# Optimization experiments

Measured on AMD Instinct MI355X. Metric: run time of the kernel, lower is better.

The kernel has to match this reference:

```python
import jax, jax.numpy as jnp
import numpy as np

DIM = 1024
NUM_HEADS = 16
HEAD_DIM = DIM // NUM_HEADS
SCALE = HEAD_DIM ** -0.5


def setup_inputs() -> dict:
    key = jax.random.key(0)
    k1, k2, k3, k4, k5 = jax.random.split(key, 5)
    B, N = 2, 2048
    h = jax.random.normal(k1, (B, N, DIM), dtype=jnp.float32)
    mask = jax.random.uniform(k2, (B, N), dtype=jnp.float32)  # non-negative, sqrt-safe
    # nn.Linear(dim, dim*3, bias=False): weight applied as x @ W^T; store as [dim, 3*dim]
    w_qkv = jax.random.normal(k3, (DIM, 3 * DIM), dtype=jnp.float32) * (DIM ** -0.5)
    w_proj = jax.random.normal(k4, (DIM, DIM), dtype=jnp.float32) * (DIM ** -0.5)
    b_proj = jax.random.normal(k5, (DIM,), dtype=jnp.float32) * 0.01
    return {"h": h, "mask": mask, "w_qkv": w_qkv, "w_proj": w_proj, "b_proj": b_proj}


def reference(h, mask, w_qkv, w_proj, b_proj):
    B, N, C = h.shape
    H, D = NUM_HEADS, HEAD_DIM
    # qkv projection -> [3, B, H, N, D]
    qkv = (h @ w_qkv).reshape(B, N, 3, H, D).transpose(2, 0, 3, 1, 4)
    q, k, v = qkv[0], qkv[1], qkv[2]
    # scores [B,H,N,N]; scale applied to logits (same math as (q@k^T)*scale)
    attn = jax.nn.softmax(jnp.einsum('bhqd,bhkd->bhqk', q, k) * SCALE, axis=-1)
    # post-softmax multiplicative mask over the KEY dimension: mask[B,N]->[B,1,1,N]
    attn = attn * mask[:, None, None, :]
    new_mask = jnp.sqrt(mask)
    out = jnp.einsum('bhqk,bhkd->bhqd', attn, v)          # [B,H,N,D]
    out = out.transpose(0, 2, 1, 3).reshape(B, N, C)       # [B,N,C]
    out = out @ w_proj + b_proj
    return out, new_mask
```

## Files before the change

kernel.cpp:

```cpp
#include <hip/hip_runtime.h>
#include <hip/hip_bf16.h>
#include <math.h>

#define DIMC   1024
#define NHEADS 16
#define HDIM   64
#define BATCH  2
#define SEQ    2048
#define SCALE  0.125f
#define QSCL   (0.125f * 1.44269504088896341f)

typedef unsigned short u16;
typedef unsigned int   u32;
typedef __attribute__((ext_vector_type(8))) short bf16x8;
typedef _Float16 f16x8 __attribute__((ext_vector_type(8)));
typedef __attribute__((ext_vector_type(4))) float f32x4;

#define BHND ((size_t)BATCH * NHEADS * SEQ * HDIM)
#define MROWS ((size_t)BATCH * SEQ)

__device__ __forceinline__ u16 f2bf(float x) {
    __hip_bfloat16 h = __float2bfloat16(x);
    return *reinterpret_cast<u16*>(&h);
}
__device__ __forceinline__ u16 f2h(float x) {
    _Float16 h = (_Float16)x;
    return *reinterpret_cast<u16*>(&h);
}
__device__ __forceinline__ u32 cvt_pk_bf16(float a, float b) {
    u32 r;
    asm("v_cvt_pk_bf16_f32 %0, %1, %2" : "=v"(r) : "v"(a), "v"(b));
    return r;
}
__device__ __forceinline__ void gload_lds16(const u16* g, u16* l) {
    __builtin_amdgcn_global_load_lds(
        (const __attribute__((address_space(1))) unsigned int*)g,
        (__attribute__((address_space(3))) unsigned int*)l, 16, 0, 0);
}

__global__ __launch_bounds__(256) void prep_h_kernel(
    const float* __restrict__ in, u16* __restrict__ outh)
{
    int i = (blockIdx.x * 256 + threadIdx.x) * 8;
    float4 a = *(const float4*)&in[i];
    float4 b = *(const float4*)&in[i + 4];
    float v[8] = {a.x, a.y, a.z, a.w, b.x, b.y, b.z, b.w};
    bf16x8 o;
    #pragma unroll
    for (int j = 0; j < 8; ++j) o[j] = (short)f2h(v[j]);
    *(bf16x8*)&outh[i] = o;
}

__global__ __launch_bounds__(256) void prep_w_kernel(
    const float* __restrict__ W, u16* __restrict__ T, int K, int N)
{
    __shared__ float Ws[64][65];
    const int kb  = blockIdx.x * 64;
    const int nb  = blockIdx.y * 64;
    const int tid = threadIdx.x;
    const int jr  = (tid & 15) * 4;
    const int ir  = tid >> 4;
    #pragma unroll
    for (int it = 0; it < 4; ++it) {
        int i = ir + it * 16;
        *(float4*)&Ws[i][jr] = *(const float4*)&W[(size_t)(kb + i) * N + nb + jr];
    }
    __syncthreads();
    const int n  = tid >> 2;
    const int k0 = (tid & 3) * 16;
    bf16x8 h0, h1;
    #pragma unroll
    for (int kk = 0; kk < 8; ++kk) {
        h0[kk] = (short)f2h(Ws[k0 + kk][n]);
        h1[kk] = (short)f2h(Ws[k0 + 8 + kk][n]);
    }
    size_t off = (size_t)(nb + n) * K + kb + k0;
    *(bf16x8*)&T[off]     = h0;
    *(bf16x8*)&T[off + 8] = h1;
}

template <int MODE>
__global__ __launch_bounds__(256) void gemm_f16_kernel(
    const u16* __restrict__ A, const u16* __restrict__ B,
    const float* __restrict__ bias, const float* __restrict__ vmask,
    float* __restrict__ outf, u16* __restrict__ outb,
    int M, int N, int K)
{
    __shared__ __align__(16) u16 lds[2][128 * 32];

    const int bm   = blockIdx.y * 128;
    const int bn   = blockIdx.x * 128;
    const int tid  = threadIdx.x;
    const int wid  = tid >> 6;
    const int lane = tid & 63;
    const int lo   = lane & 15;
    const int g4   = lane >> 4;
    const int wr   = wid >> 1, wc = wid & 1;

    const int mrow = lane >> 2;
    const int ks8  = (lane & 3) * 8;
    const u16* g0  = (wid < 2)
        ? A + (size_t)(bm + (wid & 1) * 64 + mrow) * K + ks8
        : B + (size_t)(bn + (wid & 1) * 64 + mrow) * K + ks8;
    u16* lbase = &lds[wid >> 1][(wid & 1) * 64 * 32];

    f32x4 acc[4][4] = {};

    for (int k0 = 0; k0 < K; k0 += 32) {
        const u16* g = g0 + k0;
        #pragma unroll
        for (int s = 0; s < 4; ++s)
            gload_lds16(g + (size_t)s * 16 * K, lbase + s * 512);
        __syncthreads();

        f16x8 bfr[4];
        #pragma unroll
        for (int ni = 0; ni < 4; ++ni)
            bfr[ni] = *(const f16x8*)&lds[1][(wc * 64 + ni * 16 + lo) * 32 + g4 * 8];
        #pragma unroll
        for (int mi = 0; mi < 4; ++mi) {
            f16x8 a = *(const f16x8*)&lds[0][(wr * 64 + mi * 16 + lo) * 32 + g4 * 8];
            #pragma unroll
            for (int ni = 0; ni < 4; ++ni)
                acc[mi][ni] = __builtin_amdgcn_mfma_f32_16x16x32_f16(a, bfr[ni], acc[mi][ni], 0, 0, 0);
        }
        __syncthreads();
    }

    if (MODE == 0) {
        #pragma unroll
        for (int mi = 0; mi < 4; ++mi) {
            int m0 = bm + wr * 64 + mi * 16 + 4 * g4;
            #pragma unroll
            for (int ni = 0; ni < 4; ++ni) {
                int n0    = bn + wc * 64 + ni * 16;
                int which = n0 >> 10;
                int head  = (n0 & 1023) >> 6;
                int d     = (n0 & 63) + lo;
                if (which == 0) {
                    #pragma unroll
                    for (int r = 0; r < 4; ++r) {
                        int m = m0 + r, b = m >> 11, seq = m & 2047;
                        outb[(((size_t)b * NHEADS + head) * SEQ + seq) * HDIM + d] =
                            f2bf(acc[mi][ni][r] * QSCL);
                    }
                } else if (which == 1) {
                    #pragma unroll
                    for (int r = 0; r < 4; ++r) {
                        int m = m0 + r, b = m >> 11, seq = m & 2047;
                        outb[BHND + (((size_t)b * NHEADS + head) * SEQ + seq) * HDIM + d] =
                            f2bf(acc[mi][ni][r]);
                    }
                } else {
                    int b = m0 >> 11, seq0 = m0 & 2047;
                    float4 mv = *(const float4*)&vmask[b * SEQ + seq0];
                    ushort4 o;
                    o.x = f2bf(acc[mi][ni][0] * mv.x);
                    o.y = f2bf(acc[mi][ni][1] * mv.y);
                    o.z = f2bf(acc[mi][ni][2] * mv.z);
                    o.w = f2bf(acc[mi][ni][3] * mv.w);
                    *(ushort4*)&outb[2 * BHND +
                        (((size_t)b * NHEADS + head) * HDIM + d) * SEQ + seq0] = o;
                }
            }
        }
    } else {
        #pragma unroll
        for (int ni = 0; ni < 4; ++ni) {
            int col = bn + wc * 64 + ni * 16 + lo;
            float bv = bias[col];
            #pragma unroll
            for (int mi = 0; mi < 4; ++mi) {
                int m0 = bm + wr * 64 + mi * 16 + 4 * g4;
                #pragma unroll
                for (int r = 0; r < 4; ++r)
                    outf[(size_t)(m0 + r) * N + col] = acc[mi][ni][r] + bv;
            }
        }
    }
}

__global__ __launch_bounds__(256) void attn_mfma_kernel(
    const u16* __restrict__ qb, const u16* __restrict__ kb,
    const u16* __restrict__ vtb, u16* __restrict__ oA)
{
    __shared__ __align__(16) u16 Ks[64 * 64];
    __shared__ __align__(16) u16 Vt[64 * 64];
    __shared__ __align__(16) u16 Plds[4][16 * 72];

    const int bid  = blockIdx.x;
    const int qt   = bid & 31;
    const int h    = (bid >> 5) & 15;
    const int b    = bid >> 9;
    const int tid  = threadIdx.x;
    const int wid  = tid >> 6;
    const int lane = tid & 63;
    const int lo   = lane & 15;
    const int g    = lane >> 4;

    const size_t bh = (size_t)b * NHEADS + h;
    const int qbase = qt * 64 + wid * 16;

    const u16* qrowp = qb + (bh * SEQ + qbase + lo) * HDIM + 8 * g;
    const bf16x8 aq0 = *(const bf16x8*)(qrowp);
    const bf16x8 aq1 = *(const bf16x8*)(qrowp + 32);

    const int srow  = tid >> 2;
    const int scol  = (tid & 3) * 16;
    const int swz   = (srow & 7) << 3;
    const int idx0  = srow * 64 + (scol ^ swz);
    const int idx1  = srow * 64 + ((scol + 8) ^ swz);
    const u16* kgp  = kb  + (bh * SEQ  + srow) * HDIM + scol;
    const u16* vgp  = vtb + (bh * HDIM + srow) * SEQ  + scol;

    int kof0[4], kof1[4];
    #pragma unroll
    for (int kt = 0; kt < 4; ++kt) {
        int key  = lo + 16 * kt;
        int kbse = key * 64;
        int ksw  = (key & 7) << 3;
        kof0[kt] = kbse + ((8 * g) ^ ksw);
        kof1[kt] = kbse + ((32 + 8 * g) ^ ksw);
    }
    int vof0[4], vof1[4];
    #pragma unroll
    for (int dt = 0; dt < 4; ++dt) {
        int vbse = (lo + 16 * dt) * 64;
        int vsw  = (lo & 7) << 3;
        vof0[dt] = vbse + ((8 * g) ^ vsw);
        vof1[dt] = vbse + ((32 + 8 * g) ^ vsw);
    }

    bf16x8 ones;
    #pragma unroll
    for (int j = 0; j < 8; ++j) ones[j] = (short)0x3F80;

    f32x4 acc[4] = {};
    f32x4 accl = {};

    u16* pw = &Plds[wid][0];

    bf16x8 rk0 = *(const bf16x8*)(kgp);
    bf16x8 rk1 = *(const bf16x8*)(kgp + 8);
    bf16x8 rv0 = *(const bf16x8*)(vgp);
    bf16x8 rv1 = *(const bf16x8*)(vgp + 8);

    for (int k0 = 0; k0 < SEQ; k0 += 64) {
        __syncthreads();
        *(bf16x8*)&Ks[idx0] = rk0;
        *(bf16x8*)&Ks[idx1] = rk1;
        *(bf16x8*)&Vt[idx0] = rv0;
        *(bf16x8*)&Vt[idx1] = rv1;
        __syncthreads();
        if (k0 + 64 < SEQ) {
            const u16* kn = kgp + (size_t)(k0 + 64) * HDIM;
            rk0 = *(const bf16x8*)(kn);
            rk1 = *(const bf16x8*)(kn + 8);
            rv0 = *(const bf16x8*)(vgp + k0 + 64);
            rv1 = *(const bf16x8*)(vgp + k0 + 64 + 8);
        }

        f32x4 s[4];
        #pragma unroll
        for (int kt = 0; kt < 4; ++kt) {
            f32x4 t = {};
            t = __builtin_amdgcn_mfma_f32_16x16x32_bf16(*(const bf16x8*)&Ks[kof0[kt]], aq0, t, 0, 0, 0);
            t = __builtin_amdgcn_mfma_f32_16x16x32_bf16(*(const bf16x8*)&Ks[kof1[kt]], aq1, t, 0, 0, 0);
            s[kt] = t;
        }

        #pragma unroll
        for (int kt = 0; kt < 4; ++kt) {
            uint2 pr;
            pr.x = cvt_pk_bf16(__builtin_amdgcn_exp2f(s[kt][0]),
                               __builtin_amdgcn_exp2f(s[kt][1]));
            pr.y = cvt_pk_bf16(__builtin_amdgcn_exp2f(s[kt][2]),
                               __builtin_amdgcn_exp2f(s[kt][3]));
            *(uint2*)&pw[lo * 72 + 16 * kt + 4 * g] = pr;
        }

        const bf16x8 pa0 = *(const bf16x8*)&pw[lo * 72 + 8 * g];
        const bf16x8 pa1 = *(const bf16x8*)&pw[lo * 72 + 32 + 8 * g];
        accl = __builtin_amdgcn_mfma_f32_16x16x32_bf16(pa0, ones, accl, 0, 0, 0);
        accl = __builtin_amdgcn_mfma_f32_16x16x32_bf16(pa1, ones, accl, 0, 0, 0);
        #pragma unroll
        for (int dt = 0; dt < 4; ++dt) {
            acc[dt] = __builtin_amdgcn_mfma_f32_16x16x32_bf16(pa0, *(const bf16x8*)&Vt[vof0[dt]], acc[dt], 0, 0, 0);
            acc[dt] = __builtin_amdgcn_mfma_f32_16x16x32_bf16(pa1, *(const bf16x8*)&Vt[vof1[dt]], acc[dt], 0, 0, 0);
        }
    }

    #pragma unroll
    for (int r = 0; r < 4; ++r) {
        float invq = 1.f / accl[r];
        size_t row = (size_t)b * SEQ + qbase + 4 * g + r;
        u16* dst = oA + row * DIMC + h * HDIM + lo;
        #pragma unroll
        for (int dt = 0; dt < 4; ++dt)
            dst[16 * dt] = f2h(acc[dt][r] * invq);
    }
}

__global__ void mask_sqrt_kernel(const float* __restrict__ mask,
                                 float* __restrict__ out, int n)
{
    int i = blockIdx.x * 256 + threadIdx.x;
    if (i < n) out[i] = sqrtf(mask[i]);
}

extern "C" void kernel_launch(void* const* d_in, const int* in_sizes, int n_in,
                              void* d_out, int out_size, void* d_ws, size_t ws_size,
                              hipStream_t stream)
{
    const float* h      = (const float*)d_in[0];
    const float* mask   = (const float*)d_in[1];
    const float* w_qkv  = (const float*)d_in[2];
    const float* w_proj = (const float*)d_in[3];
    const float* b_proj = (const float*)d_in[4];
    float* out = (float*)d_out;

    u16* qkv = (u16*)d_ws;
    u16* wqT = qkv + 3 * BHND;
    u16* wpT = wqT + (size_t)3072 * 1024;
    u16* hA  = wpT + (size_t)1024 * 1024;
    u16* oA  = hA;

    prep_h_kernel<<<(MROWS * DIMC) / (256 * 8), 256, 0, stream>>>(h, hA);
    prep_w_kernel<<<dim3(16, 48), 256, 0, stream>>>(w_qkv, wqT, DIMC, 3 * DIMC);
    prep_w_kernel<<<dim3(16, 16), 256, 0, stream>>>(w_proj, wpT, DIMC, DIMC);

    gemm_f16_kernel<0><<<dim3(24, 32), 256, 0, stream>>>(
        hA, wqT, nullptr, mask, nullptr, qkv, MROWS, 3 * DIMC, DIMC);

    attn_mfma_kernel<<<BATCH * NHEADS * (SEQ / 64), 256, 0, stream>>>(
        qkv, qkv + BHND, qkv + 2 * BHND, oA);

    gemm_f16_kernel<1><<<dim3(8, 32), 256, 0, stream>>>(
        oA, wpT, b_proj, nullptr, out, nullptr, MROWS, DIMC, DIMC);

    mask_sqrt_kernel<<<(BATCH * SEQ + 255) / 256, 256, 0, stream>>>(
        mask, out + MROWS * DIMC, BATCH * SEQ);
}
```

Baseline: 140.4 us.

## Merge prep launches, widen GEMM K-tile with swizzle, double-buffer attention K/V

```diff
diff --git a/kernel.cpp b/kernel.cpp
--- a/kernel.cpp
+++ b/kernel.cpp
@@ -39,24 +39,40 @@
 }
 
 __global__ __launch_bounds__(256) void prep_h_kernel(
-    const float* __restrict__ in, u16* __restrict__ outh)
-{
-    int i = (blockIdx.x * 256 + threadIdx.x) * 8;
-    float4 a = *(const float4*)&in[i];
-    float4 b = *(const float4*)&in[i + 4];
-    float v[8] = {a.x, a.y, a.z, a.w, b.x, b.y, b.z, b.w};
-    bf16x8 o;
-    #pragma unroll
-    for (int j = 0; j < 8; ++j) o[j] = (short)f2h(v[j]);
-    *(bf16x8*)&outh[i] = o;
+    const float* __restrict__ in, u16* __restrict__ outh,
+    const float* __restrict__ mask, float* __restrict__ outm)
+{
+    int bid = blockIdx.x;
+    if (bid < 2048) {
+        int i = (bid * 256 + threadIdx.x) * 8;
+        float4 a = *(const float4*)&in[i];
+        float4 b = *(const float4*)&in[i + 4];
+        float v[8] = {a.x, a.y, a.z, a.w, b.x, b.y, b.z, b.w};
+        bf16x8 o;
+        #pragma unroll
+        for (int j = 0; j < 8; ++j) o[j] = (short)f2h(v[j]);
+        *(bf16x8*)&outh[i] = o;
+    } else {
+        int i = ((bid - 2048) * 256 + threadIdx.x) * 8;
+        float4 a = *(const float4*)&mask[i];
+        float4 b = *(const float4*)&mask[i + 4];
+        float4 oa = make_float4(sqrtf(a.x), sqrtf(a.y), sqrtf(a.z), sqrtf(a.w));
+        float4 ob = make_float4(sqrtf(b.x), sqrtf(b.y), sqrtf(b.z), sqrtf(b.w));
+        *(float4*)&outm[i]     = oa;
+        *(float4*)&outm[i + 4] = ob;
+    }
 }
 
 __global__ __launch_bounds__(256) void prep_w_kernel(
-    const float* __restrict__ W, u16* __restrict__ T, int K, int N)
+    const float* __restrict__ Wq, const float* __restrict__ Wp,
+    u16* __restrict__ Tq, u16* __restrict__ Tp)
 {
     __shared__ float Ws[64][65];
+    const int K = DIMC;
+    const float* W; u16* T; int N, nb;
+    if (blockIdx.y < 48) { W = Wq; T = Tq; N = 3072; nb = blockIdx.y * 64; }
+    else                 { W = Wp; T = Tp; N = 1024; nb = (blockIdx.y - 48) * 64; }
     const int kb  = blockIdx.x * 64;
-    const int nb  = blockIdx.y * 64;
     const int tid = threadIdx.x;
     const int jr  = (tid & 15) * 4;
     const int ir  = tid >> 4;
@@ -86,7 +102,7 @@
     float* __restrict__ outf, u16* __restrict__ outb,
     int M, int N, int K)
 {
-    __shared__ __align__(16) u16 lds[2][128 * 32];
+    __shared__ __align__(16) u16 lds[2][128 * 64];
 
     const int bm   = blockIdx.y * 128;
     const int bn   = blockIdx.x * 128;
@@ -97,32 +113,36 @@
     const int g4   = lane >> 4;
     const int wr   = wid >> 1, wc = wid & 1;
 
-    const int mrow = lane >> 2;
-    const int ks8  = (lane & 3) * 8;
+    const int srow8 = lane >> 3;
+    const int scolx = 8 * ((lane & 7) ^ srow8);
     const u16* g0  = (wid < 2)
-        ? A + (size_t)(bm + (wid & 1) * 64 + mrow) * K + ks8
-        : B + (size_t)(bn + (wid & 1) * 64 + mrow) * K + ks8;
-    u16* lbase = &lds[wid >> 1][(wid & 1) * 64 * 32];
+        ? A + (size_t)(bm + (wid & 1) * 64 + srow8) * K + scolx
+        : B + (size_t)(bn + (wid & 1) * 64 + srow8) * K + scolx;
+    u16* lbase = &lds[wid >> 1][(wid & 1) * 64 * 64];
 
     f32x4 acc[4][4] = {};
 
-    for (int k0 = 0; k0 < K; k0 += 32) {
+    for (int k0 = 0; k0 < K; k0 += 64) {
         const u16* g = g0 + k0;
         #pragma unroll
-        for (int s = 0; s < 4; ++s)
-            gload_lds16(g + (size_t)s * 16 * K, lbase + s * 512);
+        for (int s = 0; s < 8; ++s)
+            gload_lds16(g + (size_t)s * 8 * K, lbase + s * 512);
         __syncthreads();
 
-        f16x8 bfr[4];
-        #pragma unroll
-        for (int ni = 0; ni < 4; ++ni)
-            bfr[ni] = *(const f16x8*)&lds[1][(wc * 64 + ni * 16 + lo) * 32 + g4 * 8];
-        #pragma unroll
-        for (int mi = 0; mi < 4; ++mi) {
-            f16x8 a = *(const f16x8*)&lds[0][(wr * 64 + mi * 16 + lo) * 32 + g4 * 8];
+        #pragma unroll
+        for (int ks = 0; ks < 2; ++ks) {
+            const int csw = 8 * ((4 * ks + g4) ^ (lo & 7));
+            f16x8 bfr[4];
             #pragma unroll
             for (int ni = 0; ni < 4; ++ni)
-                acc[mi][ni] = __builtin_amdgcn_mfma_f32_16x16x32_f16(a, bfr[ni], acc[mi][ni], 0, 0, 0);
+                bfr[ni] = *(const f16x8*)&lds[1][(wc * 64 + ni * 16 + lo) * 64 + csw];
+            #pragma unroll
+            for (int mi = 0; mi < 4; ++mi) {
+                f16x8 a = *(const f16x8*)&lds[0][(wr * 64 + mi * 16 + lo) * 64 + csw];
+                #pragma unroll
+                for (int ni = 0; ni < 4; ++ni)
+                    acc[mi][ni] = __builtin_amdgcn_mfma_f32_16x16x32_f16(a, bfr[ni], acc[mi][ni], 0, 0, 0);
+            }
         }
         __syncthreads();
     }
@@ -184,8 +204,8 @@
     const u16* __restrict__ qb, const u16* __restrict__ kb,
     const u16* __restrict__ vtb, u16* __restrict__ oA)
 {
-    __shared__ __align__(16) u16 Ks[64 * 64];
-    __shared__ __align__(16) u16 Vt[64 * 64];
+    __shared__ __align__(16) u16 Ks[2][64 * 64];
+    __shared__ __align__(16) u16 Vt[2][64 * 64];
     __shared__ __align__(16) u16 Plds[4][16 * 72];
 
     const int bid  = blockIdx.x;
@@ -239,34 +259,47 @@
     f32x4 accl = {};
 
     u16* pw = &Plds[wid][0];
+    const int NT = SEQ / 64;
 
     bf16x8 rk0 = *(const bf16x8*)(kgp);
     bf16x8 rk1 = *(const bf16x8*)(kgp + 8);
     bf16x8 rv0 = *(const bf16x8*)(vgp);
     bf16x8 rv1 = *(const bf16x8*)(vgp + 8);
-
-    for (int k0 = 0; k0 < SEQ; k0 += 64) {
-        __syncthreads();
-        *(bf16x8*)&Ks[idx0] = rk0;
-        *(bf16x8*)&Ks[idx1] = rk1;
-        *(bf16x8*)&Vt[idx0] = rv0;
-        *(bf16x8*)&Vt[idx1] = rv1;
-        __syncthreads();
-        if (k0 + 64 < SEQ) {
-            const u16* kn = kgp + (size_t)(k0 + 64) * HDIM;
-            rk0 = *(const bf16x8*)(kn);
-            rk1 = *(const bf16x8*)(kn + 8);
-            rv0 = *(const bf16x8*)(vgp + k0 + 64);
-            rv1 = *(const bf16x8*)(vgp + k0 + 64 + 8);
-        }
+    *(bf16x8*)&Ks[0][idx0] = rk0;
+    *(bf16x8*)&Ks[0][idx1] = rk1;
+    *(bf16x8*)&Vt[0][idx0] = rv0;
+    *(bf16x8*)&Vt[0][idx1] = rv1;
+    rk0 = *(const bf16x8*)(kgp + (size_t)64 * HDIM);
+    rk1 = *(const bf16x8*)(kgp + (size_t)64 * HDIM + 8);
+    rv0 = *(const bf16x8*)(vgp + 64);
+    rv1 = *(const bf16x8*)(vgp + 64 + 8);
+    __syncthreads();
+
+    for (int t = 0; t < NT; ++t) {
+        const int cur = t & 1;
+        if (t + 1 < NT) {
+            *(bf16x8*)&Ks[cur ^ 1][idx0] = rk0;
+            *(bf16x8*)&Ks[cur ^ 1][idx1] = rk1;
+            *(bf16x8*)&Vt[cur ^ 1][idx0] = rv0;
+            *(bf16x8*)&Vt[cur ^ 1][idx1] = rv1;
+            if (t + 2 < NT) {
+                const size_t k2 = (size_t)(t + 2) * 64;
+                rk0 = *(const bf16x8*)(kgp + k2 * HDIM);
+                rk1 = *(const bf16x8*)(kgp + k2 * HDIM + 8);
+                rv0 = *(const bf16x8*)(vgp + k2);
+                rv1 = *(const bf16x8*)(vgp + k2 + 8);
+            }
+        }
+        const u16* Kc = &Ks[cur][0];
+        const u16* Vc = &Vt[cur][0];
 
         f32x4 s[4];
         #pragma unroll
         for (int kt = 0; kt < 4; ++kt) {
-            f32x4 t = {};
-            t = __builtin_amdgcn_mfma_f32_16x16x32_bf16(*(const bf16x8*)&Ks[kof0[kt]], aq0, t, 0, 0, 0);
-            t = __builtin_amdgcn_mfma_f32_16x16x32_bf16(*(const bf16x8*)&Ks[kof1[kt]], aq1, t, 0, 0, 0);
-            s[kt] = t;
+            f32x4 t2 = {};
+            t2 = __builtin_amdgcn_mfma_f32_16x16x32_bf16(*(const bf16x8*)&Kc[kof0[kt]], aq0, t2, 0, 0, 0);
+            t2 = __builtin_amdgcn_mfma_f32_16x16x32_bf16(*(const bf16x8*)&Kc[kof1[kt]], aq1, t2, 0, 0, 0);
+            s[kt] = t2;
         }
 
         #pragma unroll
@@ -285,9 +318,11 @@
         accl = __builtin_amdgcn_mfma_f32_16x16x32_bf16(pa1, ones, accl, 0, 0, 0);
         #pragma unroll
         for (int dt = 0; dt < 4; ++dt) {
-            acc[dt] = __builtin_amdgcn_mfma_f32_16x16x32_bf16(pa0, *(const bf16x8*)&Vt[vof0[dt]], acc[dt], 0, 0, 0);
-            acc[dt] = __builtin_amdgcn_mfma_f32_16x16x32_bf16(pa1, *(const bf16x8*)&Vt[vof1[dt]], acc[dt], 0, 0, 0);
-        }
+            acc[dt] = __builtin_amdgcn_mfma_f32_16x16x32_bf16(pa0, *(const bf16x8*)&Vc[vof0[dt]], acc[dt], 0, 0, 0);
+            acc[dt] = __builtin_amdgcn_mfma_f32_16x16x32_bf16(pa1, *(const bf16x8*)&Vc[vof1[dt]], acc[dt], 0, 0, 0);
+        }
+
+        __syncthreads();
     }
 
     #pragma unroll
@@ -299,13 +334,6 @@
         for (int dt = 0; dt < 4; ++dt)
             dst[16 * dt] = f2h(acc[dt][r] * invq);
     }
-}
-
-__global__ void mask_sqrt_kernel(const float* __restrict__ mask,
-                                 float* __restrict__ out, int n)
-{
-    int i = blockIdx.x * 256 + threadIdx.x;
-    if (i < n) out[i] = sqrtf(mask[i]);
 }
 
 extern "C" void kernel_launch(void* const* d_in, const int* in_sizes, int n_in,
@@ -325,9 +353,8 @@
     u16* hA  = wpT + (size_t)1024 * 1024;
     u16* oA  = hA;
 
-    prep_h_kernel<<<(MROWS * DIMC) / (256 * 8), 256, 0, stream>>>(h, hA);
-    prep_w_kernel<<<dim3(16, 48), 256, 0, stream>>>(w_qkv, wqT, DIMC, 3 * DIMC);
-    prep_w_kernel<<<dim3(16, 16), 256, 0, stream>>>(w_proj, wpT, DIMC, DIMC);
+    prep_h_kernel<<<2050, 256, 0, stream>>>(h, hA, mask, out + MROWS * DIMC);
+    prep_w_kernel<<<dim3(16, 64), 256, 0, stream>>>(w_qkv, w_proj, wqT, wpT);
 
     gemm_f16_kernel<0><<<dim3(24, 32), 256, 0, stream>>>(
         hA, wqT, nullptr, mask, nullptr, qkv, MROWS, 3 * DIMC, DIMC);
@@ -337,7 +364,4 @@
 
     gemm_f16_kernel<1><<<dim3(8, 32), 256, 0, stream>>>(
         oA, wpT, b_proj, nullptr, out, nullptr, MROWS, DIMC, DIMC);
-
-    mask_sqrt_kernel<<<(BATCH * SEQ + 255) / 256, 256, 0, stream>>>(
-        mask, out + MROWS * DIMC, BATCH * SEQ);
-}
+}
```

After: 135.0 us. -3.9%, faster.
